# Kernel optimization log

Measured on AMD Instinct MI355X. Metric: run time of the kernel, lower is better.

The kernel has to match this reference:

```python
import jax, jax.numpy as jnp
import numpy as np

DIM = 1024
NUM_HEADS = 16
HEAD_DIM = DIM // NUM_HEADS
SCALE = 1.0 / float(np.sqrt(HEAD_DIM))


def setup_inputs() -> dict:
    key = jax.random.key(0)
    ks = jax.random.split(key, 8)
    b, n = 1, 4096
    x = jax.random.normal(ks[0], (b, n, DIM), dtype=jnp.float32)
    cos = jax.random.uniform(ks[1], (b, n, HEAD_DIM // 2), dtype=jnp.float32)
    sin = jax.random.uniform(ks[2], (b, n, HEAD_DIM // 2), dtype=jnp.float32)
    # qkv Linear(dim, 3*dim) and proj Linear(dim, dim); store weights as [in, out]
    w_qkv = jax.random.normal(ks[3], (DIM, 3 * DIM), dtype=jnp.float32) * (1.0 / np.sqrt(DIM))
    b_qkv = jax.random.normal(ks[4], (3 * DIM,), dtype=jnp.float32) * 0.01
    w_proj = jax.random.normal(ks[5], (DIM, DIM), dtype=jnp.float32) * (1.0 / np.sqrt(DIM))
    b_proj = jax.random.normal(ks[6], (DIM,), dtype=jnp.float32) * 0.01
    return {"x": x, "cos": cos, "sin": sin, "w_qkv": w_qkv, "b_qkv": b_qkv,
            "w_proj": w_proj, "b_proj": b_proj}


def _rotate_half(t):
    t1, t2 = jnp.split(t, 2, axis=-1)
    return jnp.concatenate([-t2, t1], axis=-1)


def reference(x, cos, sin, w_qkv, b_qkv, w_proj, b_proj):
    b, n, d = x.shape
    qkv = x @ w_qkv + b_qkv                      # [b, n, 3d]
    q, k, v = jnp.split(qkv, 3, axis=-1)
    # [b, n, h, hd] layout (avoids explicit transposes; einsum handles head axis)
    q = q.reshape(b, n, NUM_HEADS, HEAD_DIM)
    k = k.reshape(b, n, NUM_HEADS, HEAD_DIM)
    v = v.reshape(b, n, NUM_HEADS, HEAD_DIM)
    # RoPE: cos/sin [b, n, hd/2] -> [b, n, 1, hd], broadcast over heads
    cos_f = jnp.concatenate([cos, cos], axis=-1)[:, :, None, :]
    sin_f = jnp.concatenate([sin, sin], axis=-1)[:, :, None, :]
    q = q * cos_f + _rotate_half(q) * sin_f
    k = k * cos_f + _rotate_half(k) * sin_f
    # SDPA (non-causal, no dropout in eval)
    scores = jnp.einsum("bqhd,bkhd->bhqk", q, k) * SCALE
    attn = jax.nn.softmax(scores, axis=-1)
    out = jnp.einsum("bhqk,bkhd->bqhd", attn, v).reshape(b, n, d)
    return out @ w_proj + b_proj
```

## Files before the change

kernel.cpp:

```cpp
#include <hip/hip_runtime.h>
#include <hip/hip_bf16.h>
#include <cstdint>


#define TOK 4096
#define DIM_ 1024
#define NHEAD 16
#define HDIM 64
#define N3 3072
#define SCALE_LOG2E 0.18033688011112042f

typedef __bf16 bf16_t;
typedef bf16_t bf16x8 __attribute__((ext_vector_type(8)));
typedef float floatx4 __attribute__((ext_vector_type(4)));

__device__ __forceinline__ void async_ld16(const bf16_t* g, bf16_t* l) {
  __builtin_amdgcn_global_load_lds(
      (const __attribute__((address_space(1))) void*)(g),
      (__attribute__((address_space(3))) void*)(l), 16, 0, 0);
}

__global__ __launch_bounds__(256) void k_prep(
    const float* __restrict__ x, const float* __restrict__ w_qkv,
    const float* __restrict__ w_proj, bf16_t* __restrict__ xb,
    bf16_t* __restrict__ wqkvT, bf16_t* __restrict__ wprojT) {
  __shared__ float tile[32][33];
  const int b = blockIdx.x;
  if (b < 4096) {
    int i = b * 256 + threadIdx.x;
    float4 v = ((const float4*)x)[i];
    union { bf16_t bb[4]; uint64_t u; } p;
    p.bb[0] = (bf16_t)v.x; p.bb[1] = (bf16_t)v.y;
    p.bb[2] = (bf16_t)v.z; p.bb[3] = (bf16_t)v.w;
    ((uint64_t*)xb)[i] = p.u;
    return;
  }
  const float* in; bf16_t* out; int R, C, c0, r0;
  if (b < 7168) {
    int bb = b - 4096; in = w_qkv; out = wqkvT; R = 1024; C = 3072;
    c0 = (bb % 96) * 32; r0 = (bb / 96) * 32;
  } else {
    int bb = b - 7168; in = w_proj; out = wprojT; R = 1024; C = 1024;
    c0 = (bb % 32) * 32; r0 = (bb / 32) * 32;
  }
  int tx = threadIdx.x & 31, ty = threadIdx.x >> 5;
#pragma unroll
  for (int i = 0; i < 4; i++) {
    int r = ty + i * 8;
    tile[r][tx] = in[(size_t)(r0 + r) * C + c0 + tx];
  }
  __syncthreads();
#pragma unroll
  for (int i = 0; i < 4; i++) {
    int c = ty + i * 8;
    out[(size_t)(c0 + c) * R + r0 + tx] = (bf16_t)tile[tx][c];
  }
}

__global__ __launch_bounds__(256) void k_qkv(
    const bf16_t* __restrict__ A,
    const bf16_t* __restrict__ Bt,
    const float* __restrict__ bias,
    const float* __restrict__ cs,
    const float* __restrict__ sn,
    bf16_t* __restrict__ qb, bf16_t* __restrict__ kb, bf16_t* __restrict__ vT) {
  constexpr int K = 1024, BK = 32;
  __shared__ bf16_t As[128 * BK] __attribute__((aligned(16)));
  __shared__ bf16_t Bs[128 * BK] __attribute__((aligned(16)));
  const int t = threadIdx.x;
  const int lane = t & 63, w = t >> 6;
  const int lrow = lane & 15, quad = lane >> 4;
  const int m0 = blockIdx.y * 128, n0 = blockIdx.x * 128;
  const int wm = (w >> 1) * 64, wn = (w & 1) * 64;

  const floatx4 ZV = {0.f, 0.f, 0.f, 0.f};
  floatx4 acc[4][4];
#pragma unroll
  for (int i = 0; i < 4; i++)
#pragma unroll
    for (int j = 0; j < 4; j++) acc[i][j] = ZV;

  for (int kt = 0; kt < K; kt += BK) {
#pragma unroll
    for (int r = 0; r < 2; r++) {
      int idx = r * 256 + t;
      int lbase = (r * 256 + w * 64) * 8;
      async_ld16(&A[(size_t)(m0 + (idx >> 2)) * K + kt + (idx & 3) * 8], &As[lbase]);
      async_ld16(&Bt[(size_t)(n0 + (idx >> 2)) * K + kt + (idx & 3) * 8], &Bs[lbase]);
    }
    __syncthreads();
    bf16x8 af[4], bf[4];
#pragma unroll
    for (int i = 0; i < 4; i++)
      af[i] = *(const bf16x8*)&As[(wm + i * 16 + lrow) * BK + quad * 8];
#pragma unroll
    for (int i = 0; i < 4; i++)
      bf[i] = *(const bf16x8*)&Bs[(wn + i * 16 + lrow) * BK + quad * 8];
#pragma unroll
    for (int mi = 0; mi < 4; mi++)
#pragma unroll
      for (int ni = 0; ni < 4; ni++)
        acc[mi][ni] = __builtin_amdgcn_mfma_f32_16x16x32_bf16(af[mi], bf[ni], acc[mi][ni], 0, 0, 0);
    __syncthreads();
  }

  const int c0 = n0 + wn;
  const int seg = c0 >> 10;
  const int h = (c0 & 1023) >> 6;
  float bv[4];
#pragma unroll
  for (int ni = 0; ni < 4; ni++) bv[ni] = bias[c0 + ni * 16 + lrow];

  if (seg < 2) {
    bf16_t* base = ((seg == 0) ? qb : kb) + (size_t)h * TOK * HDIM;
    const float qs = (seg == 0) ? SCALE_LOG2E : 1.0f;
#pragma unroll
    for (int mi = 0; mi < 4; mi++) {
#pragma unroll
      for (int reg = 0; reg < 4; reg++) {
        const int r = m0 + wm + mi * 16 + quad * 4 + reg;
        const float c_lo = cs[r * 32 + lrow];
        const float c_hi = cs[r * 32 + 16 + lrow];
        const float s_lo = sn[r * 32 + lrow];
        const float s_hi = sn[r * 32 + 16 + lrow];
        const float v0 = acc[mi][0][reg] + bv[0];
        const float v1 = acc[mi][1][reg] + bv[1];
        const float v2 = acc[mi][2][reg] + bv[2];
        const float v3 = acc[mi][3][reg] + bv[3];
        const float o0 = (v0 * c_lo - v2 * s_lo) * qs;
        const float o1 = (v1 * c_hi - v3 * s_hi) * qs;
        const float o2 = (v2 * c_lo + v0 * s_lo) * qs;
        const float o3 = (v3 * c_hi + v1 * s_hi) * qs;
        bf16_t* rp = base + (size_t)r * HDIM + lrow;
        rp[0]  = (bf16_t)o0;
        rp[16] = (bf16_t)o1;
        rp[32] = (bf16_t)o2;
        rp[48] = (bf16_t)o3;
      }
    }
  } else {
    bf16_t* base = vT + (size_t)h * HDIM * TOK;
#pragma unroll
    for (int mi = 0; mi < 4; mi++) {
      const int rbase = m0 + wm + mi * 16 + quad * 4;
#pragma unroll
      for (int ni = 0; ni < 4; ni++) {
        union { bf16_t b[4]; uint64_t u; } p;
#pragma unroll
        for (int reg = 0; reg < 4; reg++) p.b[reg] = (bf16_t)(acc[mi][ni][reg] + bv[ni]);
        *(uint64_t*)&base[(size_t)(ni * 16 + lrow) * TOK + rbase] = p.u;
      }
    }
  }
}

__global__ __launch_bounds__(256, 2) void k_attn(
    const bf16_t* __restrict__ qb, const bf16_t* __restrict__ kb,
    const bf16_t* __restrict__ vT, bf16_t* __restrict__ ao) {
  __shared__ bf16_t Ks[2][64 * 64] __attribute__((aligned(16)));
  __shared__ bf16_t Vs[2][64 * 64] __attribute__((aligned(16)));
  __shared__ bf16_t Ps[4][64 * 36] __attribute__((aligned(16)));
  const int t = threadIdx.x, lane = t & 63, w = t >> 6;
  const int lrow = lane & 15, quad = lane >> 4;
  const int qg = w & 1, kh = w >> 1;
  const int h = blockIdx.x & 15;
  const int q0 = (blockIdx.x >> 4) * 128;
  const bf16_t* qh = qb + (size_t)h * TOK * HDIM;
  const bf16_t* khp = kb + (size_t)h * TOK * HDIM;
  const bf16_t* vhp = vT + (size_t)h * HDIM * TOK;
  bf16_t* Pw = &Ps[w][0];

  const int ksrc = (t >> 3) * HDIM + (((t & 7) ^ ((t >> 3) & 7)) * 8);
  const int vsrc = (t >> 3) * TOK + (((t & 7) ^ ((t >> 3) & 7)) * 8);

  bf16x8 qf[4][2];
#pragma unroll
  for (int ni = 0; ni < 4; ni++)
#pragma unroll
    for (int ks = 0; ks < 2; ks++)
      qf[ni][ks] = *(const bf16x8*)&qh[(size_t)(q0 + qg * 64 + ni * 16 + lrow) * HDIM + ks * 32 + quad * 8];

  const floatx4 ZV = {0.f, 0.f, 0.f, 0.f};
  floatx4 o[4][4];
  floatx4 lacc[4] = {ZV, ZV, ZV, ZV};
#pragma unroll
  for (int d = 0; d < 4; d++)
#pragma unroll
    for (int ni = 0; ni < 4; ni++) o[d][ni] = ZV;

#pragma unroll
  for (int r = 0; r < 2; r++) {
    async_ld16(&khp[(size_t)(r * 32) * HDIM + ksrc], &Ks[0][r * 2048 + t * 8]);
    async_ld16(&vhp[(size_t)(r * 32) * TOK + vsrc], &Vs[0][r * 2048 + t * 8]);
  }

  for (int it = 0; it < TOK / 64; ++it) {
    const int b = it & 1;
    __syncthreads();
    if (it + 1 < TOK / 64) {
      const int j1 = (it + 1) * 64;
#pragma unroll
      for (int r = 0; r < 2; r++) {
        async_ld16(&khp[((size_t)j1 + r * 32) * HDIM + ksrc], &Ks[b ^ 1][r * 2048 + t * 8]);
        async_ld16(&vhp[(size_t)(r * 32) * TOK + j1 + vsrc], &Vs[b ^ 1][r * 2048 + t * 8]);
      }
    }

    floatx4 s[2][4];
#pragma unroll
    for (int mi = 0; mi < 2; mi++)
#pragma unroll
      for (int ni = 0; ni < 4; ni++) s[mi][ni] = ZV;
#pragma unroll
    for (int ks = 0; ks < 2; ks++)
#pragma unroll
      for (int mi = 0; mi < 2; mi++) {
        bf16x8 kf = *(const bf16x8*)&Ks[b][(kh * 32 + mi * 16 + lrow) * 64 + (((ks * 4 + quad) ^ (lrow & 7)) * 8)];
#pragma unroll
        for (int ni = 0; ni < 4; ni++)
          s[mi][ni] = __builtin_amdgcn_mfma_f32_16x16x32_bf16(kf, qf[ni][ks], s[mi][ni], 0, 0, 0);
      }

#pragma unroll
    for (int mi = 0; mi < 2; mi++)
#pragma unroll
      for (int ni = 0; ni < 4; ni++) {
#pragma unroll
        for (int reg = 0; reg < 4; reg++)
          s[mi][ni][reg] = __builtin_amdgcn_exp2f(s[mi][ni][reg]);
        lacc[ni] += s[mi][ni];
      }

#pragma unroll
    for (int mi = 0; mi < 2; mi++)
#pragma unroll
      for (int ni = 0; ni < 4; ni++) {
        union { bf16_t b4[4]; uint64_t u; } p;
#pragma unroll
        for (int reg = 0; reg < 4; reg++) p.b4[reg] = (bf16_t)s[mi][ni][reg];
        *(uint64_t*)&Pw[(ni * 16 + lrow) * 36 + (mi * 4 + quad) * 4] = p.u;
      }

    bf16x8 pf[4];
#pragma unroll
    for (int ni = 0; ni < 4; ni++) {
      const int row = (ni * 16 + lrow) * 36;
      union { uint64_t u[2]; bf16x8 v; } pp;
      pp.u[0] = *(const uint64_t*)&Pw[row + quad * 8];
      pp.u[1] = *(const uint64_t*)&Pw[row + quad * 8 + 4];
      pf[ni] = pp.v;
    }
#pragma unroll
    for (int dt = 0; dt < 4; dt++) {
      bf16x8 vf = *(const bf16x8*)&Vs[b][(dt * 16 + lrow) * 64 + (((kh * 4 + quad) ^ (lrow & 7)) * 8)];
#pragma unroll
      for (int ni = 0; ni < 4; ni++)
        o[dt][ni] = __builtin_amdgcn_mfma_f32_16x16x32_bf16(vf, pf[ni], o[dt][ni], 0, 0, 0);
    }
  }

  __syncthreads();
  float* Mrg = (qg == 0) ? (float*)&Ks[0][0] : (float*)&Vs[0][0];
  float* Lmrg = (float*)&Ps[0][0];
  float lq[4];
#pragma unroll
  for (int ni = 0; ni < 4; ni++) {
    float l = lacc[ni][0] + lacc[ni][1] + lacc[ni][2] + lacc[ni][3];
    l += __shfl_xor(l, 16, 64);
    l += __shfl_xor(l, 32, 64);
    lq[ni] = l;
  }
  if (kh == 1) {
#pragma unroll
    for (int ni = 0; ni < 4; ni++) {
#pragma unroll
      for (int dt = 0; dt < 4; dt++)
        *(floatx4*)&Mrg[(ni * 16 + lrow) * 64 + dt * 16 + quad * 4] = o[dt][ni];
      if (quad == 0) Lmrg[qg * 64 + ni * 16 + lrow] = lq[ni];
    }
  }
  __syncthreads();
  if (kh == 0) {
#pragma unroll
    for (int ni = 0; ni < 4; ni++) {
      const float l = lq[ni] + Lmrg[qg * 64 + ni * 16 + lrow];
      const float inv = 1.0f / l;
      const int qrow = q0 + qg * 64 + ni * 16 + lrow;
#pragma unroll
      for (int dt = 0; dt < 4; dt++) {
        floatx4 ov = *(const floatx4*)&Mrg[(ni * 16 + lrow) * 64 + dt * 16 + quad * 4];
        union { bf16_t b4[4]; uint64_t u; } p;
#pragma unroll
        for (int reg = 0; reg < 4; reg++) p.b4[reg] = (bf16_t)((o[dt][ni][reg] + ov[reg]) * inv);
        *(uint64_t*)&ao[(size_t)qrow * DIM_ + h * HDIM + dt * 16 + quad * 4] = p.u;
      }
    }
  }
}

__global__ __launch_bounds__(256) void k_proj(
    const bf16_t* __restrict__ A,
    const bf16_t* __restrict__ Bt,
    const float* __restrict__ bias, float* __restrict__ out) {
  constexpr int K = 1024, BK = 32;
  __shared__ bf16_t As[64 * BK] __attribute__((aligned(16)));
  __shared__ bf16_t Bs[128 * BK] __attribute__((aligned(16)));
  const int t = threadIdx.x;
  const int lane = t & 63, w = t >> 6;
  const int lrow = lane & 15, quad = lane >> 4;
  const int m0 = blockIdx.y * 64, n0 = blockIdx.x * 128;
  const int wm = (w >> 1) * 32, wn = (w & 1) * 64;

  const floatx4 ZV = {0.f, 0.f, 0.f, 0.f};
  floatx4 acc[2][4];
#pragma unroll
  for (int i = 0; i < 2; i++)
#pragma unroll
    for (int j = 0; j < 4; j++) acc[i][j] = ZV;

  for (int kt = 0; kt < K; kt += BK) {
    async_ld16(&A[(size_t)(m0 + (t >> 2)) * K + kt + (t & 3) * 8], &As[w * 512]);
#pragma unroll
    for (int r = 0; r < 2; r++) {
      int idx = r * 256 + t;
      async_ld16(&Bt[(size_t)(n0 + (idx >> 2)) * K + kt + (idx & 3) * 8],
                 &Bs[(r * 256 + w * 64) * 8]);
    }
    __syncthreads();
    bf16x8 af[2], bf[4];
#pragma unroll
    for (int i = 0; i < 2; i++)
      af[i] = *(const bf16x8*)&As[(wm + i * 16 + lrow) * BK + quad * 8];
#pragma unroll
    for (int i = 0; i < 4; i++)
      bf[i] = *(const bf16x8*)&Bs[(wn + i * 16 + lrow) * BK + quad * 8];
#pragma unroll
    for (int mi = 0; mi < 2; mi++)
#pragma unroll
      for (int ni = 0; ni < 4; ni++)
        acc[mi][ni] = __builtin_amdgcn_mfma_f32_16x16x32_bf16(af[mi], bf[ni], acc[mi][ni], 0, 0, 0);
    __syncthreads();
  }

  const int c0 = n0 + wn;
#pragma unroll
  for (int ni = 0; ni < 4; ni++) {
    float bv = bias[c0 + ni * 16 + lrow];
#pragma unroll
    for (int mi = 0; mi < 2; mi++)
#pragma unroll
      for (int reg = 0; reg < 4; reg++) {
        int r = m0 + wm + mi * 16 + quad * 4 + reg;
        out[(size_t)r * DIM_ + c0 + ni * 16 + lrow] = acc[mi][ni][reg] + bv;
      }
  }
}

extern "C" void kernel_launch(void* const* d_in, const int* in_sizes, int n_in,
                              void* d_out, int out_size, void* d_ws, size_t ws_size,
                              hipStream_t stream) {
  const float* x      = (const float*)d_in[0];
  const float* cs     = (const float*)d_in[1];
  const float* sn     = (const float*)d_in[2];
  const float* w_qkv  = (const float*)d_in[3];
  const float* b_qkv  = (const float*)d_in[4];
  const float* w_proj = (const float*)d_in[5];
  const float* b_proj = (const float*)d_in[6];
  float* out = (float*)d_out;

  char* ws = (char*)d_ws;
  bf16_t* xb     = (bf16_t*)(ws);
  bf16_t* wqkvT  = (bf16_t*)(ws + 8388608);
  bf16_t* wprojT = (bf16_t*)(ws + 14680064);
  bf16_t* qb     = (bf16_t*)(ws + 16777216);
  bf16_t* kb     = (bf16_t*)(ws + 25165824);
  bf16_t* vT     = (bf16_t*)(ws + 33554432);
  bf16_t* ao     = xb;

  k_prep<<<dim3(8192), dim3(256), 0, stream>>>(x, w_qkv, w_proj, xb, wqkvT, wprojT);
  k_qkv<<<dim3(24, 32), dim3(256), 0, stream>>>(xb, wqkvT, b_qkv, cs, sn, qb, kb, vT);
  k_attn<<<dim3(512), dim3(256), 0, stream>>>(qb, kb, vT, ao);
  k_proj<<<dim3(8, 64), dim3(256), 0, stream>>>(ao, wprojT, b_proj, out);
}
```

Before: 221.9 us.

## Halve attention query tile, load V directly to registers, raise occupancy

The attention kernel now handles 64 query rows per block instead of 128, doubling the grid to 1024 blocks and raising the launch-bounds occupancy target from 2 to 4 blocks per CU. V tiles are no longer staged through double-buffered shared memory; each wave loads its V fragments straight from global memory every iteration. The block index is also remapped so neighbouring blocks take different heads. This cuts LDS use and register pressure to allow more waves in flight, but every block re-reads K and V, doubling total K/V traffic, and the direct global V loads are not prefetched.

```diff
diff --git a/kernel.cpp b/kernel.cpp
--- a/kernel.cpp
+++ b/kernel.cpp
@@ -154,77 +154,77 @@
   }
 }
 
-__global__ __launch_bounds__(256, 2) void k_attn(
+__global__ __launch_bounds__(256, 4) void k_attn(
     const bf16_t* __restrict__ qb, const bf16_t* __restrict__ kb,
     const bf16_t* __restrict__ vT, bf16_t* __restrict__ ao) {
   __shared__ bf16_t Ks[2][64 * 64] __attribute__((aligned(16)));
-  __shared__ bf16_t Vs[2][64 * 64] __attribute__((aligned(16)));
-  __shared__ bf16_t Ps[4][64 * 36] __attribute__((aligned(16)));
+  __shared__ bf16_t Ps[4][32 * 36] __attribute__((aligned(16)));
   const int t = threadIdx.x, lane = t & 63, w = t >> 6;
   const int lrow = lane & 15, quad = lane >> 4;
   const int qg = w & 1, kh = w >> 1;
-  const int h = blockIdx.x & 15;
-  const int q0 = (blockIdx.x >> 4) * 128;
+  const int bx = blockIdx.x;
+  const int h = ((bx & 7) << 1) | ((bx >> 3) & 1);
+  const int q0 = (bx >> 4) * 64;
   const bf16_t* qh = qb + (size_t)h * TOK * HDIM;
   const bf16_t* khp = kb + (size_t)h * TOK * HDIM;
   const bf16_t* vhp = vT + (size_t)h * HDIM * TOK;
   bf16_t* Pw = &Ps[w][0];
 
   const int ksrc = (t >> 3) * HDIM + (((t & 7) ^ ((t >> 3) & 7)) * 8);
-  const int vsrc = (t >> 3) * TOK + (((t & 7) ^ ((t >> 3) & 7)) * 8);
-
-  bf16x8 qf[4][2];
-#pragma unroll
-  for (int ni = 0; ni < 4; ni++)
+
+  bf16x8 qf[2][2];
+#pragma unroll
+  for (int ni = 0; ni < 2; ni++)
 #pragma unroll
     for (int ks = 0; ks < 2; ks++)
-      qf[ni][ks] = *(const bf16x8*)&qh[(size_t)(q0 + qg * 64 + ni * 16 + lrow) * HDIM + ks * 32 + quad * 8];
+      qf[ni][ks] = *(const bf16x8*)&qh[(size_t)(q0 + qg * 32 + ni * 16 + lrow) * HDIM + ks * 32 + quad * 8];
 
   const floatx4 ZV = {0.f, 0.f, 0.f, 0.f};
-  floatx4 o[4][4];
-  floatx4 lacc[4] = {ZV, ZV, ZV, ZV};
+  floatx4 o[4][2];
+  floatx4 lacc[2] = {ZV, ZV};
 #pragma unroll
   for (int d = 0; d < 4; d++)
 #pragma unroll
-    for (int ni = 0; ni < 4; ni++) o[d][ni] = ZV;
-
-#pragma unroll
-  for (int r = 0; r < 2; r++) {
+    for (int ni = 0; ni < 2; ni++) o[d][ni] = ZV;
+
+#pragma unroll
+  for (int r = 0; r < 2; r++)
     async_ld16(&khp[(size_t)(r * 32) * HDIM + ksrc], &Ks[0][r * 2048 + t * 8]);
-    async_ld16(&vhp[(size_t)(r * 32) * TOK + vsrc], &Vs[0][r * 2048 + t * 8]);
-  }
 
   for (int it = 0; it < TOK / 64; ++it) {
     const int b = it & 1;
     __syncthreads();
     if (it + 1 < TOK / 64) {
-      const int j1 = (it + 1) * 64;
-#pragma unroll
-      for (int r = 0; r < 2; r++) {
-        async_ld16(&khp[((size_t)j1 + r * 32) * HDIM + ksrc], &Ks[b ^ 1][r * 2048 + t * 8]);
-        async_ld16(&vhp[(size_t)(r * 32) * TOK + j1 + vsrc], &Vs[b ^ 1][r * 2048 + t * 8]);
-      }
-    }
-
-    floatx4 s[2][4];
-#pragma unroll
-    for (int mi = 0; mi < 2; mi++)
-#pragma unroll
-      for (int ni = 0; ni < 4; ni++) s[mi][ni] = ZV;
+      const size_t j1 = (size_t)(it + 1) * 64;
+#pragma unroll
+      for (int r = 0; r < 2; r++)
+        async_ld16(&khp[(j1 + r * 32) * HDIM + ksrc], &Ks[b ^ 1][r * 2048 + t * 8]);
+    }
+
+    bf16x8 vf[4];
+#pragma unroll
+    for (int dt = 0; dt < 4; dt++)
+      vf[dt] = *(const bf16x8*)&vhp[(size_t)(dt * 16 + lrow) * TOK + it * 64 + kh * 32 + quad * 8];
+
+    floatx4 s[2][2];
+#pragma unroll
+    for (int mi = 0; mi < 2; mi++)
+#pragma unroll
+      for (int ni = 0; ni < 2; ni++) s[mi][ni] = ZV;
 #pragma unroll
     for (int ks = 0; ks < 2; ks++)
 #pragma unroll
       for (int mi = 0; mi < 2; mi++) {
         bf16x8 kf = *(const bf16x8*)&Ks[b][(kh * 32 + mi * 16 + lrow) * 64 + (((ks * 4 + quad) ^ (lrow & 7)) * 8)];
 #pragma unroll
-        for (int ni = 0; ni < 4; ni++)
+        for (int ni = 0; ni < 2; ni++)
           s[mi][ni] = __builtin_amdgcn_mfma_f32_16x16x32_bf16(kf, qf[ni][ks], s[mi][ni], 0, 0, 0);
       }
 
 #pragma unroll
     for (int mi = 0; mi < 2; mi++)
 #pragma unroll
-      for (int ni = 0; ni < 4; ni++) {
+      for (int ni = 0; ni < 2; ni++) {
 #pragma unroll
         for (int reg = 0; reg < 4; reg++)
           s[mi][ni][reg] = __builtin_amdgcn_exp2f(s[mi][ni][reg]);
@@ -234,16 +234,16 @@
 #pragma unroll
     for (int mi = 0; mi < 2; mi++)
 #pragma unroll
-      for (int ni = 0; ni < 4; ni++) {
+      for (int ni = 0; ni < 2; ni++) {
         union { bf16_t b4[4]; uint64_t u; } p;
 #pragma unroll
         for (int reg = 0; reg < 4; reg++) p.b4[reg] = (bf16_t)s[mi][ni][reg];
         *(uint64_t*)&Pw[(ni * 16 + lrow) * 36 + (mi * 4 + quad) * 4] = p.u;
       }
 
-    bf16x8 pf[4];
-#pragma unroll
-    for (int ni = 0; ni < 4; ni++) {
+    bf16x8 pf[2];
+#pragma unroll
+    for (int ni = 0; ni < 2; ni++) {
       const int row = (ni * 16 + lrow) * 36;
       union { uint64_t u[2]; bf16x8 v; } pp;
       pp.u[0] = *(const uint64_t*)&Pw[row + quad * 8];
@@ -251,20 +251,18 @@
       pf[ni] = pp.v;
     }
 #pragma unroll
-    for (int dt = 0; dt < 4; dt++) {
-      bf16x8 vf = *(const bf16x8*)&Vs[b][(dt * 16 + lrow) * 64 + (((kh * 4 + quad) ^ (lrow & 7)) * 8)];
-#pragma unroll
-      for (int ni = 0; ni < 4; ni++)
-        o[dt][ni] = __builtin_amdgcn_mfma_f32_16x16x32_bf16(vf, pf[ni], o[dt][ni], 0, 0, 0);
-    }
+    for (int dt = 0; dt < 4; dt++)
+#pragma unroll
+      for (int ni = 0; ni < 2; ni++)
+        o[dt][ni] = __builtin_amdgcn_mfma_f32_16x16x32_bf16(vf[dt], pf[ni], o[dt][ni], 0, 0, 0);
   }
 
   __syncthreads();
-  float* Mrg = (qg == 0) ? (float*)&Ks[0][0] : (float*)&Vs[0][0];
+  float* Mrg = (float*)&Ks[qg][0];
   float* Lmrg = (float*)&Ps[0][0];
-  float lq[4];
-#pragma unroll
-  for (int ni = 0; ni < 4; ni++) {
+  float lq[2];
+#pragma unroll
+  for (int ni = 0; ni < 2; ni++) {
     float l = lacc[ni][0] + lacc[ni][1] + lacc[ni][2] + lacc[ni][3];
     l += __shfl_xor(l, 16, 64);
     l += __shfl_xor(l, 32, 64);
@@ -272,20 +270,20 @@
   }
   if (kh == 1) {
 #pragma unroll
-    for (int ni = 0; ni < 4; ni++) {
+    for (int ni = 0; ni < 2; ni++) {
 #pragma unroll
       for (int dt = 0; dt < 4; dt++)
         *(floatx4*)&Mrg[(ni * 16 + lrow) * 64 + dt * 16 + quad * 4] = o[dt][ni];
-      if (quad == 0) Lmrg[qg * 64 + ni * 16 + lrow] = lq[ni];
+      if (quad == 0) Lmrg[qg * 32 + ni * 16 + lrow] = lq[ni];
     }
   }
   __syncthreads();
   if (kh == 0) {
 #pragma unroll
-    for (int ni = 0; ni < 4; ni++) {
-      const float l = lq[ni] + Lmrg[qg * 64 + ni * 16 + lrow];
+    for (int ni = 0; ni < 2; ni++) {
+      const float l = lq[ni] + Lmrg[qg * 32 + ni * 16 + lrow];
       const float inv = 1.0f / l;
-      const int qrow = q0 + qg * 64 + ni * 16 + lrow;
+      const int qrow = q0 + qg * 32 + ni * 16 + lrow;
 #pragma unroll
       for (int dt = 0; dt < 4; dt++) {
         floatx4 ov = *(const floatx4*)&Mrg[(ni * 16 + lrow) * 64 + dt * 16 + quad * 4];
@@ -379,6 +377,6 @@
 
   k_prep<<<dim3(8192), dim3(256), 0, stream>>>(x, w_qkv, w_proj, xb, wqkvT, wprojT);
   k_qkv<<<dim3(24, 32), dim3(256), 0, stream>>>(xb, wqkvT, b_qkv, cs, sn, qb, kb, vT);
-  k_attn<<<dim3(512), dim3(256), 0, stream>>>(qb, kb, vT, ao);
+  k_attn<<<dim3(1024), dim3(256), 0, stream>>>(qb, kb, vT, ao);
   k_proj<<<dim3(8, 64), dim3(256), 0, stream>>>(ao, wprojT, b_proj, out);
 }
```

New measurement: 277.0 us. 1.25x slower.
